# Optimization experiments

Hardware: AMD Instinct MI355X
Metric: run time of the kernel (lower is better)

## Reference

```python
import jax, jax.numpy as jnp
import numpy as np

B, S = 4, 128          # batch, seq
IN, OUT = 1024, 1024   # perfect squares
C = 256                # compressed_feature_dim
K = 4                  # num_monarchs
NI, NO = 32, 32        # sqrt(IN), sqrt(OUT)
D1 = NI * NI * NO      # flat size of M1 per token
D2 = NO * NI * NO      # flat size of M2 per token


def setup_inputs() -> dict:
    key = jax.random.key(0)
    ks = jax.random.split(key, 20)
    s = 0.02
    return {
        "x":   jax.random.normal(ks[0], (B, S, IN), dtype=jnp.float32),
        # compressor: Linear(IN, C)
        "Wc":  jax.random.normal(ks[1], (IN, C), dtype=jnp.float32) * s,
        "bc":  jnp.zeros((C,), dtype=jnp.float32),
        # M1 generators (stacked over K experts): Linear(C,C), SiLU, Linear(C,D1)
        "W1a": jax.random.normal(ks[2], (K, C, C), dtype=jnp.float32) * s,
        "b1a": jnp.zeros((K, C), dtype=jnp.float32),
        "W1b": jax.random.normal(ks[3], (K, C, D1), dtype=jnp.float32) * s,
        "b1b": jax.random.normal(ks[4], (K, D1), dtype=jnp.float32) * s,
        # M2 generators
        "W2a": jax.random.normal(ks[5], (K, C, C), dtype=jnp.float32) * s,
        "b2a": jnp.zeros((K, C), dtype=jnp.float32),
        "W2b": jax.random.normal(ks[6], (K, C, D2), dtype=jnp.float32) * s,
        "b2b": jax.random.normal(ks[7], (K, D2), dtype=jnp.float32) * s,
        # mixer: Linear(C,C), SiLU, Linear(C,K)
        "Wm1": jax.random.normal(ks[8], (C, C), dtype=jnp.float32) * s,
        "bm1": jnp.zeros((C,), dtype=jnp.float32),
        "Wm2": jax.random.normal(ks[9], (C, K), dtype=jnp.float32) * s,
        "bm2": jnp.zeros((K,), dtype=jnp.float32),
        # biasor: Linear(C, OUT)
        "Wb":  jax.random.normal(ks[10], (C, OUT), dtype=jnp.float32) * s,
        "bb":  jnp.zeros((OUT,), dtype=jnp.float32),
        # ratio_gen: Linear(C, 1)
        "Wr":  jax.random.normal(ks[11], (C, 1), dtype=jnp.float32) * s,
        "br":  jnp.ones((1,), dtype=jnp.float32),
    }


def reference(x, Wc, bc, W1a, b1a, W1b, b1b, W2a, b2a, W2b, b2b,
              Wm1, bm1, Wm2, bm2, Wb, bb, Wr, br):
    silu = jax.nn.silu
    # compressor
    c = silu(x @ Wc + bc)                                   # [B,S,C]
    # per-expert hypernetwork generation of flat Monarch factors
    h1 = silu(jnp.einsum('bsc,kcd->kbsd', c, W1a) + b1a[:, None, None, :])
    M1s = jnp.einsum('kbsd,kde->kbse', h1, W1b) + b1b[:, None, None, :]  # [K,B,S,D1]
    h2 = silu(jnp.einsum('bsc,kcd->kbsd', c, W2a) + b2a[:, None, None, :])
    M2s = jnp.einsum('kbsd,kde->kbse', h2, W2b) + b2b[:, None, None, :]  # [K,B,S,D2]
    # softmax mixing coefficients
    coeffs = jax.nn.softmax(silu(c @ Wm1 + bm1) @ Wm2 + bm2, axis=-1)    # [B,S,K]
    M1_flat = jnp.einsum('kbsd,bsk->bsd', M1s, coeffs)      # [B,S,D1]
    M2_flat = jnp.einsum('kbsd,bsk->bsd', M2s, coeffs)      # [B,S,D2]
    # per-token Monarch matmul
    lead = x.shape[:-1]
    M1 = M1_flat.reshape(*lead, NI, NI, NO)
    M2 = M2_flat.reshape(*lead, NO, NI, NO)
    x1 = x.reshape(*lead, NI, NI)                            # [B,S,g=NI,i=NI]
    x1o = jnp.einsum('bsgi,bsgio->bsgo', x1, M1)             # [B,S,NI,NO]
    x2 = jnp.swapaxes(x1o, -1, -2)                           # [B,S,NO,NI]
    x2o = jnp.einsum('bsgi,bsgio->bsgo', x2, M2)             # [B,S,NO,NO]
    y = x2o.reshape(*lead, NO * NO)                          # [B,S,OUT]
    ratio = c @ Wr + br                                      # [B,S,1]
    return y * ratio + (c @ Wb + bb)
```

## Files before the change

kernel.cpp:

```cpp
#include <hip/hip_runtime.h>


typedef __bf16 bf16x8 __attribute__((ext_vector_type(8)));
typedef __bf16 bf16x2 __attribute__((ext_vector_type(2)));
typedef float  fx4    __attribute__((ext_vector_type(4)));

#define NN 32768

__device__ __forceinline__ unsigned short f2bf(float f) {
  union { __bf16 b; unsigned short u; } c; c.b = (__bf16)f; return c.u;
}
__device__ __forceinline__ unsigned pk2(float lo, float hi) {
  bf16x2 v; v[0] = (__bf16)lo; v[1] = (__bf16)hi;
  union { bf16x2 v; unsigned u; } c; c.v = v; return c.u;
}
__device__ __forceinline__ float b2f(unsigned short s) {
  union { unsigned u; float f; } v; v.u = ((unsigned)s) << 16; return v.f;
}
__device__ __forceinline__ void up8(uint4 h, float* f) {
  f[0] = b2f((unsigned short)(h.x & 0xFFFF)); f[1] = b2f((unsigned short)(h.x >> 16));
  f[2] = b2f((unsigned short)(h.y & 0xFFFF)); f[3] = b2f((unsigned short)(h.y >> 16));
  f[4] = b2f((unsigned short)(h.z & 0xFFFF)); f[5] = b2f((unsigned short)(h.z >> 16));
  f[6] = b2f((unsigned short)(h.w & 0xFFFF)); f[7] = b2f((unsigned short)(h.w >> 16));
}
__device__ __forceinline__ uint4 scale8(uint4 h, float cv) {
  uint4 u;
  u.x = pk2(b2f((unsigned short)(h.x & 0xFFFF)) * cv, b2f((unsigned short)(h.x >> 16)) * cv);
  u.y = pk2(b2f((unsigned short)(h.y & 0xFFFF)) * cv, b2f((unsigned short)(h.y >> 16)) * cv);
  u.z = pk2(b2f((unsigned short)(h.z & 0xFFFF)) * cv, b2f((unsigned short)(h.z >> 16)) * cv);
  u.w = pk2(b2f((unsigned short)(h.w & 0xFFFF)) * cv, b2f((unsigned short)(h.w >> 16)) * cv);
  return u;
}
__device__ __forceinline__ float silu_f(float x) { return x / (1.f + __expf(-x)); }

__device__ __forceinline__ void gl2lds16(const void* g, void* l) {
  __builtin_amdgcn_global_load_lds(
      (const __attribute__((address_space(1))) unsigned int*)g,
      (__attribute__((address_space(3))) unsigned int*)l, 16, 0, 0);
}

#define MFMA(a, b, c) __builtin_amdgcn_mfma_f32_16x16x32_bf16((a), (b), (c), 0, 0, 0)

__global__ __launch_bounds__(256) void k1_compress(
    const float* __restrict__ x, const float* __restrict__ Wc,
    const float* __restrict__ bc, uint4* __restrict__ c_u4) {
  const int tid = threadIdx.x;
  const int m0 = blockIdx.x * 64, n0 = blockIdx.y * 64;
  __shared__ uint4 As[8 * 64];
  __shared__ uint4 Bs[8 * 65];
  const bf16x8* Af = reinterpret_cast<const bf16x8*>(As);
  const bf16x8* Bf = reinterpret_cast<const bf16x8*>(Bs);
  uint2* Bs2 = reinterpret_cast<uint2*>(Bs);
  const int lane = tid & 63, w = tid >> 6;
  const int q = lane >> 4, rr = lane & 15;
  const int wm = (w >> 1) * 32, wn = (w & 1) * 32;
  const int arun = tid & 7, amb = tid >> 3;
  const int kgrp = tid & 15, colg = tid >> 4;
  fx4 a00 = 0, a01 = 0, a10 = 0, a11 = 0;
  fx4 areg[4], breg[4];

#pragma unroll
  for (int s = 0; s < 2; ++s) {
    const float* src = x + (size_t)(m0 + amb + 32 * s) * 1024 + arun * 8;
    areg[2 * s] = *(const fx4*)src;
    areg[2 * s + 1] = *(const fx4*)(src + 4);
  }
#pragma unroll
  for (int kk = 0; kk < 4; ++kk)
    breg[kk] = *(const fx4*)(Wc + (size_t)(kgrp * 4 + kk) * 256 + n0 + colg * 4);

  for (int kt = 0; kt < 16; ++kt) {
    __syncthreads();
#pragma unroll
    for (int s = 0; s < 2; ++s) {
      uint4 u;
      u.x = pk2(areg[2 * s][0], areg[2 * s][1]);
      u.y = pk2(areg[2 * s][2], areg[2 * s][3]);
      u.z = pk2(areg[2 * s + 1][0], areg[2 * s + 1][1]);
      u.w = pk2(areg[2 * s + 1][2], areg[2 * s + 1][3]);
      As[arun * 64 + amb + 32 * s] = u;
    }
#pragma unroll
    for (int j = 0; j < 4; ++j) {
      uint2 u;
      u.x = pk2(breg[0][j], breg[1][j]);
      u.y = pk2(breg[2][j], breg[3][j]);
      Bs2[(((kgrp >> 1) * 65 + colg * 4 + j) << 1) + (kgrp & 1)] = u;
    }
    __syncthreads();
    if (kt < 15) {
      const int k0 = (kt + 1) * 64;
#pragma unroll
      for (int s = 0; s < 2; ++s) {
        const float* src = x + (size_t)(m0 + amb + 32 * s) * 1024 + k0 + arun * 8;
        areg[2 * s] = *(const fx4*)src;
        areg[2 * s + 1] = *(const fx4*)(src + 4);
      }
#pragma unroll
      for (int kk = 0; kk < 4; ++kk)
        breg[kk] = *(const fx4*)(Wc + (size_t)(k0 + kgrp * 4 + kk) * 256 + n0 + colg * 4);
    }
#pragma unroll
    for (int ks = 0; ks < 2; ++ks) {
      const int roA = (ks * 4 + q) * 64, roB = (ks * 4 + q) * 65;
      bf16x8 fa0 = Af[roA + wm + rr];
      bf16x8 fa1 = Af[roA + wm + 16 + rr];
      bf16x8 fb0 = Bf[roB + wn + rr];
      bf16x8 fb1 = Bf[roB + wn + 16 + rr];
      a00 = MFMA(fa0, fb0, a00); a01 = MFMA(fa0, fb1, a01);
      a10 = MFMA(fa1, fb0, a10); a11 = MFMA(fa1, fb1, a11);
    }
  }
  __syncthreads();
  {
    const int r4 = tid >> 6, m = tid & 63;
    uint4 u; u.x = (r4 == 0) ? 0x3F80u : 0u; u.y = 0; u.z = 0; u.w = 0;
    As[r4 * 64 + m] = u;
    uint4 ub; ub.x = (r4 == 0) ? (unsigned)f2bf(bc[n0 + m]) : 0u;
    ub.y = 0; ub.z = 0; ub.w = 0;
    Bs[r4 * 65 + m] = ub;
  }
  __syncthreads();
  {
    bf16x8 fa0 = Af[q * 64 + wm + rr];
    bf16x8 fa1 = Af[q * 64 + wm + 16 + rr];
    bf16x8 fb0 = Bf[q * 65 + wn + rr];
    bf16x8 fb1 = Bf[q * 65 + wn + 16 + rr];
    a00 = MFMA(fa0, fb0, a00); a01 = MFMA(fa0, fb1, a01);
    a10 = MFMA(fa1, fb0, a10); a11 = MFMA(fa1, fb1, a11);
  }
  unsigned short* c16 = (unsigned short*)c_u4;
#pragma unroll
  for (int fi = 0; fi < 2; ++fi) {
#pragma unroll
    for (int fj = 0; fj < 2; ++fj) {
      fx4 v = (fi == 0) ? (fj == 0 ? a00 : a01) : (fj == 0 ? a10 : a11);
      const int cc = n0 + wn + fj * 16 + rr;
#pragma unroll
      for (int reg = 0; reg < 4; ++reg) {
        const int t = m0 + wm + fi * 16 + q * 4 + reg;
        c16[((size_t)(cc >> 3) * 512 + t) * 8 + (cc & 7)] = f2bf(silu_f(v[reg]));
      }
    }
  }
  if (blockIdx.y == 0) {
    const int r4 = tid >> 6, m = tid & 63;
    uint4 u; u.x = (r4 == 0) ? 0x3F80u : 0u; u.y = 0; u.z = 0; u.w = 0;
    c_u4[(size_t)(32 + r4) * 512 + m0 + m] = u;
  }
}

__global__ __launch_bounds__(256) void k2_hyper(
    const uint4* __restrict__ c_u4,
    const float* __restrict__ W1a, const float* __restrict__ b1a,
    const float* __restrict__ W2a, const float* __restrict__ b2a,
    const float* __restrict__ Wm1, const float* __restrict__ bm1,
    const float* __restrict__ Wb, const float* __restrict__ bb,
    unsigned short* __restrict__ H, float* __restrict__ biasout) {
  const int tid = threadIdx.x;
  const int m0 = blockIdx.x * 64, n0 = blockIdx.y * 64;
  __shared__ uint4 As[2][8 * 64];
  __shared__ uint4 Bs[8 * 65];
  const bf16x8* Bf = reinterpret_cast<const bf16x8*>(Bs);
  uint2* Bs2 = reinterpret_cast<uint2*>(Bs);
  const int lane = tid & 63, w = tid >> 6;
  const int q = lane >> 4, rr = lane & 15;
  const int wm = (w >> 1) * 32, wn = (w & 1) * 32;
  const int kgrp = tid & 15, colg = tid >> 4;

  const float* bbase; const float* biasv; int bstride;
  if (n0 < 1024) {
    const int kx = n0 >> 8;
    bbase = W1a + (size_t)kx * 65536 + (n0 & 255); bstride = 256;
    biasv = b1a + kx * 256 + (n0 & 255);
  } else if (n0 < 2048) {
    const int mm = n0 - 1024; const int kx = mm >> 8;
    bbase = W2a + (size_t)kx * 65536 + (mm & 255); bstride = 256;
    biasv = b2a + kx * 256 + (mm & 255);
  } else if (n0 < 2304) {
    bbase = Wm1 + (n0 - 2048); bstride = 256; biasv = bm1 + (n0 - 2048);
  } else {
    bbase = Wb + (n0 - 2304); bstride = 1024; biasv = bb + (n0 - 2304);
  }

  fx4 a00 = 0, a01 = 0, a10 = 0, a11 = 0;
  fx4 breg[4];
#pragma unroll
  for (int kk = 0; kk < 4; ++kk)
    breg[kk] = *(const fx4*)(bbase + (size_t)(kgrp * 4 + kk) * bstride + colg * 4);
#pragma unroll
  for (int s = 0; s < 2; ++s) {
    const int run = w * 2 + s;
    gl2lds16(c_u4 + (size_t)run * 512 + m0 + lane, (void*)(&As[0][run * 64]));
  }
  int cur = 0;
  for (int kt = 0; kt < 4; ++kt) {
    __syncthreads();
#pragma unroll
    for (int j = 0; j < 4; ++j) {
      uint2 u;
      u.x = pk2(breg[0][j], breg[1][j]);
      u.y = pk2(breg[2][j], breg[3][j]);
      Bs2[(((kgrp >> 1) * 65 + colg * 4 + j) << 1) + (kgrp & 1)] = u;
    }
    __syncthreads();
    if (kt < 3) {
#pragma unroll
      for (int s = 0; s < 2; ++s) {
        const int run = w * 2 + s;
        gl2lds16(c_u4 + (size_t)((kt + 1) * 8 + run) * 512 + m0 + lane,
                 (void*)(&As[cur ^ 1][run * 64]));
      }
#pragma unroll
      for (int kk = 0; kk < 4; ++kk)
        breg[kk] = *(const fx4*)(bbase + (size_t)((kt + 1) * 64 + kgrp * 4 + kk) * bstride + colg * 4);
    }
    const bf16x8* Af = reinterpret_cast<const bf16x8*>(As[cur]);
#pragma unroll
    for (int ks = 0; ks < 2; ++ks) {
      const int roA = (ks * 4 + q) * 64, roB = (ks * 4 + q) * 65;
      bf16x8 fa0 = Af[roA + wm + rr];
      bf16x8 fa1 = Af[roA + wm + 16 + rr];
      bf16x8 fb0 = Bf[roB + wn + rr];
      bf16x8 fb1 = Bf[roB + wn + 16 + rr];
      a00 = MFMA(fa0, fb0, a00); a01 = MFMA(fa0, fb1, a01);
      a10 = MFMA(fa1, fb0, a10); a11 = MFMA(fa1, fb1, a11);
    }
    cur ^= 1;
  }
  __syncthreads();
  {
    gl2lds16(c_u4 + (size_t)(32 + w) * 512 + m0 + lane, (void*)(&As[0][w * 64]));
    const int r4 = tid >> 6, col = tid & 63;
    uint4 ub; ub.x = (r4 == 0) ? (unsigned)f2bf(biasv[col]) : 0u;
    ub.y = 0; ub.z = 0; ub.w = 0;
    Bs[r4 * 65 + col] = ub;
  }
  __syncthreads();
  {
    const bf16x8* Af = reinterpret_cast<const bf16x8*>(As[0]);
    bf16x8 fa0 = Af[q * 64 + wm + rr];
    bf16x8 fa1 = Af[q * 64 + wm + 16 + rr];
    bf16x8 fb0 = Bf[q * 65 + wn + rr];
    bf16x8 fb1 = Bf[q * 65 + wn + 16 + rr];
    a00 = MFMA(fa0, fb0, a00); a01 = MFMA(fa0, fb1, a01);
    a10 = MFMA(fa1, fb0, a10); a11 = MFMA(fa1, fb1, a11);
  }
#pragma unroll
  for (int fi = 0; fi < 2; ++fi) {
#pragma unroll
    for (int fj = 0; fj < 2; ++fj) {
      fx4 v = (fi == 0) ? (fj == 0 ? a00 : a01) : (fj == 0 ? a10 : a11);
      const int cc = n0 + wn + fj * 16 + rr;
#pragma unroll
      for (int reg = 0; reg < 4; ++reg) {
        const int t = m0 + wm + fi * 16 + q * 4 + reg;
        if (n0 < 2304)
          H[(((size_t)(cc >> 3) * 512 + t) << 3) + (cc & 7)] = f2bf(silu_f(v[reg]));
        else
          biasout[(size_t)t * 1024 + (cc - 2304)] = v[reg];
      }
    }
  }
}

__global__ __launch_bounds__(256) void k3_prep(
    const uint4* __restrict__ Hu, const uint4* __restrict__ c_u4,
    const float* __restrict__ Wm2, const float* __restrict__ bm2,
    const float* __restrict__ Wr, const float* __restrict__ br,
    uint4* __restrict__ G1u, uint4* __restrict__ G2u, float* __restrict__ ratio) {
  const int tid = threadIdx.x;
  const int tg = blockIdx.x & 7, dgrp = blockIdx.x >> 3;
  const int t0 = tg * 64;
  __shared__ float sWm2[1024];
  __shared__ float sWr[256];
  __shared__ float part[64][4][4];
  __shared__ float rp[64][4];
  __shared__ float cf[64][4];
  ((fx4*)sWm2)[tid] = ((const fx4*)Wm2)[tid];
  if (tid < 64) ((fx4*)sWr)[tid] = ((const fx4*)Wr)[tid];
  __syncthreads();
  const int tl = tid >> 2, kx = tid & 3;
  {
    float pe0 = 0, pe1 = 0, pe2 = 0, pe3 = 0, pr = 0;
#pragma unroll
    for (int i = 0; i < 8; ++i) {
      uint4 h  = Hu[(size_t)(256 + kx * 8 + i) * 512 + t0 + tl];
      uint4 cu = c_u4[(size_t)(kx * 8 + i) * 512 + t0 + tl];
      float hf[8], cv[8];
      up8(h, hf); up8(cu, cv);
#pragma unroll
      for (int j = 0; j < 8; ++j) {
        const int ch = kx * 64 + i * 8 + j;
        pe0 += hf[j] * sWm2[ch * 4 + 0];
        pe1 += hf[j] * sWm2[ch * 4 + 1];
        pe2 += hf[j] * sWm2[ch * 4 + 2];
        pe3 += hf[j] * sWm2[ch * 4 + 3];
        pr  += cv[j] * sWr[ch];
      }
    }
    part[tl][kx][0] = pe0; part[tl][kx][1] = pe1;
    part[tl][kx][2] = pe2; part[tl][kx][3] = pe3;
    rp[tl][kx] = pr;
  }
  __syncthreads();
  if (tid < 64) {
    float l[4];
#pragma unroll
    for (int e = 0; e < 4; ++e)
      l[e] = part[tid][0][e] + part[tid][1][e] + part[tid][2][e] + part[tid][3][e] + bm2[e];
    float m = fmaxf(fmaxf(l[0], l[1]), fmaxf(l[2], l[3]));
    float e0 = __expf(l[0] - m), e1 = __expf(l[1] - m);
    float e2 = __expf(l[2] - m), e3 = __expf(l[3] - m);
    float den = e0 + e1 + e2 + e3;
    cf[tid][0] = e0 / den; cf[tid][1] = e1 / den;
    cf[tid][2] = e2 / den; cf[tid][3] = e3 / den;
    if (dgrp == 0)
      ratio[t0 + tid] = rp[tid][0] + rp[tid][1] + rp[tid][2] + rp[tid][3] + br[0];
  }
  __syncthreads();
  const int tl2 = tid & 63, sub = tid >> 6;
#pragma unroll
  for (int i = 0; i < 4; ++i) {
    const int dg = dgrp * 16 + sub * 4 + i;
    const float cv = cf[tl2][dg >> 5];
    uint4 h1 = Hu[(size_t)dg * 512 + t0 + tl2];
    G1u[(size_t)dg * 512 + t0 + tl2] = scale8(h1, cv);
    uint4 h2 = Hu[(size_t)(128 + dg) * 512 + t0 + tl2];
    G2u[(size_t)dg * 512 + t0 + tl2] = scale8(h2, cv);
  }
  if (dgrp == 0) {
    if (tid < 64) {
      uint4 u;
      u.x = pk2(cf[tid][0], cf[tid][1]);
      u.y = pk2(cf[tid][2], cf[tid][3]);
      u.z = 0; u.w = 0;
      G1u[(size_t)128 * 512 + t0 + tid] = u;
      G2u[(size_t)128 * 512 + t0 + tid] = u;
    } else {
      const int idx = tid - 64;
      uint4 z; z.x = 0; z.y = 0; z.z = 0; z.w = 0;
      G1u[(size_t)(129 + (idx >> 6)) * 512 + t0 + (idx & 63)] = z;
      G2u[(size_t)(129 + (idx >> 6)) * 512 + t0 + (idx & 63)] = z;
    }
  }
}

__global__ __launch_bounds__(256) void k_biggemm(
    const uint4* __restrict__ Gu, const float* __restrict__ W,
    const float* __restrict__ bvec, unsigned short* __restrict__ Mout) {
  const int tid = threadIdx.x;
  const int p = blockIdx.x;
  const int xcd = p & 7, slot = p >> 3;
  const int m0 = (slot & 3) * 128;
  const int n0 = ((slot >> 2) * 8 + xcd) * 128;
  __shared__ uint4 Bs[2][8 * 129];
  const int lane = tid & 63, w = tid >> 6;
  const int q = lane >> 4, rr = lane & 15;
  const int wm = (w >> 1) * 64, wn = (w & 1) * 64;
  const int bcg = tid >> 3;
  const int br  = tid & 7;
  const float* wptr = W + n0 + bcg * 4;
  const uint4* aptr = Gu + m0 + wm + rr;

  fx4 acc[4][4];
#pragma unroll
  for (int i = 0; i < 4; ++i)
#pragma unroll
    for (int j = 0; j < 4; ++j) acc[i][j] = 0;

  fx4 breg[8];
  uint4 a_cur[4], a_nxt[4];
#pragma unroll
  for (int kk = 0; kk < 8; ++kk)
    breg[kk] = *(const fx4*)(wptr + (size_t)(br * 8 + kk) * NN);
#pragma unroll
  for (int j = 0; j < 4; ++j) {
    uint4 u;
    u.x = pk2(breg[0][j], breg[1][j]); u.y = pk2(breg[2][j], breg[3][j]);
    u.z = pk2(breg[4][j], breg[5][j]); u.w = pk2(breg[6][j], breg[7][j]);
    Bs[0][br * 129 + bcg * 4 + j] = u;
  }
#pragma unroll
  for (int kk = 0; kk < 8; ++kk)
    breg[kk] = *(const fx4*)(wptr + (size_t)(64 + br * 8 + kk) * NN);
#pragma unroll
  for (int f = 0; f < 4; ++f) a_cur[f] = aptr[(size_t)q * 512 + f * 16];
  __syncthreads();

  for (int kt = 0; kt < 16; ++kt) {
    const int cur = kt & 1;
    const bf16x8* Bf = reinterpret_cast<const bf16x8*>(Bs[cur]);
    if (kt < 15) {
#pragma unroll
      for (int j = 0; j < 4; ++j) {
        uint4 u;
        u.x = pk2(breg[0][j], breg[1][j]); u.y = pk2(breg[2][j], breg[3][j]);
        u.z = pk2(breg[4][j], breg[5][j]); u.w = pk2(breg[6][j], breg[7][j]);
        Bs[cur ^ 1][br * 129 + bcg * 4 + j] = u;
      }
      if (kt < 14) {
#pragma unroll
        for (int kk = 0; kk < 8; ++kk)
          breg[kk] = *(const fx4*)(wptr + (size_t)((kt + 2) * 64 + br * 8 + kk) * NN);
      }
    }
#pragma unroll
    for (int ks = 0; ks < 2; ++ks) {
      if (kt < 15 || ks < 1) {
        const int nk8 = (ks == 0) ? (kt * 8 + 4 + q) : ((kt + 1) * 8 + q);
#pragma unroll
        for (int f = 0; f < 4; ++f) a_nxt[f] = aptr[(size_t)nk8 * 512 + f * 16];
      }
      bf16x8 b[4];
      const int roB = (ks * 4 + q) * 129;
#pragma unroll
      for (int f = 0; f < 4; ++f) b[f] = Bf[roB + wn + f * 16 + rr];
#pragma unroll
      for (int fi = 0; fi < 4; ++fi) {
        bf16x8 af = *reinterpret_cast<bf16x8*>(&a_cur[fi]);
#pragma unroll
        for (int fj = 0; fj < 4; ++fj) acc[fi][fj] = MFMA(af, b[fj], acc[fi][fj]);
      }
#pragma unroll
      for (int f = 0; f < 4; ++f) a_cur[f] = a_nxt[f];
    }
    __syncthreads();
  }
  {
#pragma unroll
    for (int f = 0; f < 4; ++f) a_cur[f] = aptr[(size_t)(128 + q) * 512 + f * 16];
    const int colB = tid & 127, half = tid >> 7;
    if (half == 0) {
#pragma unroll
      for (int r = 0; r < 4; ++r) {
        float v8[8];
#pragma unroll
        for (int j = 0; j < 8; ++j) {
          const int kk = r * 8 + j;
          v8[j] = (kk < 4) ? bvec[(size_t)kk * NN + n0 + colB] : 0.f;
        }
        uint4 u; u.x = pk2(v8[0], v8[1]); u.y = pk2(v8[2], v8[3]);
        u.z = pk2(v8[4], v8[5]); u.w = pk2(v8[6], v8[7]);
        Bs[0][r * 129 + colB] = u;
      }
    }
    __syncthreads();
    const bf16x8* Bf0 = reinterpret_cast<const bf16x8*>(Bs[0]);
    bf16x8 b[4];
#pragma unroll
    for (int f = 0; f < 4; ++f) b[f] = Bf0[q * 129 + wn + f * 16 + rr];
#pragma unroll
    for (int fi = 0; fi < 4; ++fi) {
      bf16x8 af = *reinterpret_cast<bf16x8*>(&a_cur[fi]);
#pragma unroll
      for (int fj = 0; fj < 4; ++fj) acc[fi][fj] = MFMA(af, b[fj], acc[fi][fj]);
    }
  }
#pragma unroll
  for (int fi = 0; fi < 4; ++fi) {
    const int tb = m0 + wm + fi * 16 + q * 4;
#pragma unroll
    for (int fj = 0; fj < 4; ++fj) {
      const fx4 v = acc[fi][fj];
      const int cc = n0 + wn + fj * 16 + rr;
      const int pc = ((cc >> 5) & 31) * 1024 + (cc >> 10) * 32 + (cc & 31);
#pragma unroll
      for (int reg = 0; reg < 4; ++reg)
        Mout[(size_t)(tb + reg) * NN + pc] = f2bf(v[reg]);
    }
  }
}

__global__ __launch_bounds__(256) void k_monarch1(
    const float* __restrict__ x, const unsigned short* __restrict__ M1p,
    float* __restrict__ XT) {
  const int tt = blockIdx.x, tid = threadIdx.x;
  const int h = tid >> 7, t2 = tid & 127;
  __shared__ float xs[1024];
  __shared__ float xo[2][1024];
  *(float4*)&xs[tid * 4] = *(const float4*)&x[(size_t)tt * 1024 + tid * 4];
  __syncthreads();
  const int g = t2 >> 2, ob = (t2 & 3) * 8;
  const unsigned short* mrow =
      M1p + (size_t)tt * NN + (size_t)h * 16 * 1024 + g * 32 + ob;
  float acc[8] = {0, 0, 0, 0, 0, 0, 0, 0};
#pragma unroll
  for (int i = 0; i < 16; ++i) {
    uint4 mv = *(const uint4*)&mrow[(size_t)i * 1024];
    float mf[8]; up8(mv, mf);
    const float xv = xs[g * 32 + h * 16 + i];
#pragma unroll
    for (int j = 0; j < 8; ++j) acc[j] += xv * mf[j];
  }
#pragma unroll
  for (int j = 0; j < 8; ++j) xo[h][(ob + j) * 32 + g] = acc[j];
  __syncthreads();
  {
    const int base = tid * 4;
    float4 v0 = *(const float4*)&xo[0][base];
    float4 v1 = *(const float4*)&xo[1][base];
    float4 o; o.x = v0.x + v1.x; o.y = v0.y + v1.y;
    o.z = v0.z + v1.z; o.w = v0.w + v1.w;
    *(float4*)&XT[(size_t)tt * 1024 + base] = o;
  }
}

__global__ __launch_bounds__(256) void k_monarch2(
    const unsigned short* __restrict__ M2p, const float* __restrict__ XT,
    const float* __restrict__ biasout, const float* __restrict__ ratio,
    float* __restrict__ out) {
  const int tt = blockIdx.x, tid = threadIdx.x;
  const int h = tid >> 7, t2 = tid & 127;
  __shared__ float xs[1024];
  __shared__ float xo[2][1024];
  *(float4*)&xs[tid * 4] = *(const float4*)&XT[(size_t)tt * 1024 + tid * 4];
  __syncthreads();
  const int g = t2 >> 2, ob = (t2 & 3) * 8;
  const unsigned short* mrow =
      M2p + (size_t)tt * NN + (size_t)h * 16 * 1024 + g * 32 + ob;
  float acc[8] = {0, 0, 0, 0, 0, 0, 0, 0};
#pragma unroll
  for (int i = 0; i < 16; ++i) {
    uint4 mv = *(const uint4*)&mrow[(size_t)i * 1024];
    float mf[8]; up8(mv, mf);
    const float xv = xs[g * 32 + h * 16 + i];
#pragma unroll
    for (int j = 0; j < 8; ++j) acc[j] += xv * mf[j];
  }
#pragma unroll
  for (int j = 0; j < 8; ++j) xo[h][g * 32 + ob + j] = acc[j];
  __syncthreads();
  {
    const float r = ratio[tt];
    const int base = tid * 4;
    float4 v0 = *(const float4*)&xo[0][base];
    float4 v1 = *(const float4*)&xo[1][base];
    float4 bo = *(const float4*)&biasout[(size_t)tt * 1024 + base];
    float4 o;
    o.x = (v0.x + v1.x) * r + bo.x; o.y = (v0.y + v1.y) * r + bo.y;
    o.z = (v0.z + v1.z) * r + bo.z; o.w = (v0.w + v1.w) * r + bo.w;
    *(float4*)&out[(size_t)tt * 1024 + base] = o;
  }
}

extern "C" void kernel_launch(void* const* d_in, const int* in_sizes, int n_in,
                              void* d_out, int out_size, void* d_ws, size_t ws_size,
                              hipStream_t stream) {
  (void)in_sizes; (void)n_in; (void)out_size; (void)ws_size;
  const float* x   = (const float*)d_in[0];
  const float* Wc  = (const float*)d_in[1];
  const float* bc  = (const float*)d_in[2];
  const float* W1a = (const float*)d_in[3];
  const float* b1a = (const float*)d_in[4];
  const float* W1b = (const float*)d_in[5];
  const float* b1b = (const float*)d_in[6];
  const float* W2a = (const float*)d_in[7];
  const float* b2a = (const float*)d_in[8];
  const float* W2b = (const float*)d_in[9];
  const float* b2b = (const float*)d_in[10];
  const float* Wm1 = (const float*)d_in[11];
  const float* bm1 = (const float*)d_in[12];
  const float* Wm2 = (const float*)d_in[13];
  const float* bm2 = (const float*)d_in[14];
  const float* Wb  = (const float*)d_in[15];
  const float* bb  = (const float*)d_in[16];
  const float* Wr  = (const float*)d_in[17];
  const float* br  = (const float*)d_in[18];
  float* out = (float*)d_out;

  char* ws = (char*)d_ws;
  uint4* c_u4            = (uint4*)(ws + 0);
  unsigned short* H      = (unsigned short*)(ws + 294912);
  float* biasout         = (float*)(ws + 2654208);
  uint4* G1u             = (uint4*)(ws + 4751360);
  uint4* G2u             = (uint4*)(ws + 5832704);
  float* ratio           = (float*)(ws + 6914048);
  float* XT              = (float*)(ws + 6918144);
  unsigned short* M      = (unsigned short*)(ws + 9015296);

  k1_compress<<<dim3(8, 4), 256, 0, stream>>>(x, Wc, bc, c_u4);
  k2_hyper<<<dim3(8, 52), 256, 0, stream>>>(c_u4, W1a, b1a, W2a, b2a, Wm1, bm1,
                                            Wb, bb, H, biasout);
  k3_prep<<<64, 256, 0, stream>>>((const uint4*)H, c_u4, Wm2, bm2, Wr, br,
                                  G1u, G2u, ratio);
  k_biggemm<<<1024, 256, 0, stream>>>(G1u, W1b, b1b, M);
  k_monarch1<<<512, 256, 0, stream>>>(x, M, XT);
  k_biggemm<<<1024, 256, 0, stream>>>(G2u, W2b, b2b, M);
  k_monarch2<<<512, 256, 0, stream>>>(M, XT, biasout, ratio, out);
}
```

Baseline: 468.6 us.

## Pre-convert generator weights to bf16 in piggybacked blocks, use direct-to-LDS loads in biggemm

The fp32-to-bf16 packing of W1b/W2b (and their biases) moves out of the big GEMM into extra blocks appended to k1_compress and k_monarch1. Those blocks write a pre-packed bf16 workspace Wt that the GEMM then streams with global_load_lds. The GEMM loses its register-staged B pipeline and the in-loop conversions, and each K step now loads A and B tiles straight into LDS between two barriers. The trade-off is an extra full write and read of the converted weights each call, plus a GEMM with no software double-buffering.

```diff
diff --git a/kernel.cpp b/kernel.cpp
--- a/kernel.cpp
+++ b/kernel.cpp
@@ -41,11 +41,43 @@
 
 #define MFMA(a, b, c) __builtin_amdgcn_mfma_f32_16x16x32_bf16((a), (b), (c), 0, 0, 0)
 
+__device__ __forceinline__ void wconv_body(int cb, const float* __restrict__ W,
+                                           const float* __restrict__ bvec,
+                                           uint4* __restrict__ Wt) {
+  const int ur = cb >> 5;
+  const int n0 = (cb & 31) * 1024 + threadIdx.x * 4;
+  fx4 r[8];
+  if (ur < 128) {
+#pragma unroll
+    for (int kk = 0; kk < 8; ++kk)
+      r[kk] = *(const fx4*)(W + (size_t)(ur * 8 + kk) * NN + n0);
+  } else {
+#pragma unroll
+    for (int kk = 0; kk < 8; ++kk) r[kk] = 0;
+    if (ur == 128) {
+#pragma unroll
+      for (int kk = 0; kk < 4; ++kk)
+        r[kk] = *(const fx4*)(bvec + (size_t)kk * NN + n0);
+    }
+  }
+#pragma unroll
+  for (int j = 0; j < 4; ++j) {
+    uint4 u;
+    u.x = pk2(r[0][j], r[1][j]); u.y = pk2(r[2][j], r[3][j]);
+    u.z = pk2(r[4][j], r[5][j]); u.w = pk2(r[6][j], r[7][j]);
+    Wt[(size_t)ur * NN + n0 + j] = u;
+  }
+}
+
 __global__ __launch_bounds__(256) void k1_compress(
     const float* __restrict__ x, const float* __restrict__ Wc,
-    const float* __restrict__ bc, uint4* __restrict__ c_u4) {
+    const float* __restrict__ bc, uint4* __restrict__ c_u4,
+    const float* __restrict__ W1b, const float* __restrict__ b1b,
+    uint4* __restrict__ Wt) {
+  const int b = blockIdx.x;
+  if (b >= 32) { wconv_body(b - 32, W1b, b1b, Wt); return; }
   const int tid = threadIdx.x;
-  const int m0 = blockIdx.x * 64, n0 = blockIdx.y * 64;
+  const int m0 = (b & 7) * 64, n0 = (b >> 3) * 64;
   __shared__ uint4 As[8 * 64];
   __shared__ uint4 Bs[8 * 65];
   const bf16x8* Af = reinterpret_cast<const bf16x8*>(As);
@@ -143,7 +175,7 @@
       }
     }
   }
-  if (blockIdx.y == 0) {
+  if ((b >> 3) == 0) {
     const int r4 = tid >> 6, m = tid & 63;
     uint4 u; u.x = (r4 == 0) ? 0x3F80u : 0u; u.y = 0; u.z = 0; u.w = 0;
     c_u4[(size_t)(32 + r4) * 512 + m0 + m] = u;
@@ -347,21 +379,20 @@
 }
 
 __global__ __launch_bounds__(256) void k_biggemm(
-    const uint4* __restrict__ Gu, const float* __restrict__ W,
-    const float* __restrict__ bvec, unsigned short* __restrict__ Mout) {
+    const uint4* __restrict__ Gu, const uint4* __restrict__ Wt,
+    unsigned short* __restrict__ Mout) {
   const int tid = threadIdx.x;
   const int p = blockIdx.x;
   const int xcd = p & 7, slot = p >> 3;
   const int m0 = (slot & 3) * 128;
   const int n0 = ((slot >> 2) * 8 + xcd) * 128;
-  __shared__ uint4 Bs[2][8 * 129];
+  __shared__ uint4 As[8 * 128];
+  __shared__ uint4 Bs[8 * 128];
+  const bf16x8* Af = reinterpret_cast<const bf16x8*>(As);
+  const bf16x8* Bf = reinterpret_cast<const bf16x8*>(Bs);
   const int lane = tid & 63, w = tid >> 6;
   const int q = lane >> 4, rr = lane & 15;
   const int wm = (w >> 1) * 64, wn = (w & 1) * 64;
-  const int bcg = tid >> 3;
-  const int br  = tid & 7;
-  const float* wptr = W + n0 + bcg * 4;
-  const uint4* aptr = Gu + m0 + wm + rr;
 
   fx4 acc[4][4];
 #pragma unroll
@@ -369,93 +400,56 @@
 #pragma unroll
     for (int j = 0; j < 4; ++j) acc[i][j] = 0;
 
-  fx4 breg[8];
-  uint4 a_cur[4], a_nxt[4];
-#pragma unroll
-  for (int kk = 0; kk < 8; ++kk)
-    breg[kk] = *(const fx4*)(wptr + (size_t)(br * 8 + kk) * NN);
-#pragma unroll
-  for (int j = 0; j < 4; ++j) {
-    uint4 u;
-    u.x = pk2(breg[0][j], breg[1][j]); u.y = pk2(breg[2][j], breg[3][j]);
-    u.z = pk2(breg[4][j], breg[5][j]); u.w = pk2(breg[6][j], breg[7][j]);
-    Bs[0][br * 129 + bcg * 4 + j] = u;
-  }
-#pragma unroll
-  for (int kk = 0; kk < 8; ++kk)
-    breg[kk] = *(const fx4*)(wptr + (size_t)(64 + br * 8 + kk) * NN);
-#pragma unroll
-  for (int f = 0; f < 4; ++f) a_cur[f] = aptr[(size_t)q * 512 + f * 16];
-  __syncthreads();
-
   for (int kt = 0; kt < 16; ++kt) {
-    const int cur = kt & 1;
-    const bf16x8* Bf = reinterpret_cast<const bf16x8*>(Bs[cur]);
-    if (kt < 15) {
-#pragma unroll
-      for (int j = 0; j < 4; ++j) {
-        uint4 u;
-        u.x = pk2(breg[0][j], breg[1][j]); u.y = pk2(breg[2][j], breg[3][j]);
-        u.z = pk2(breg[4][j], breg[5][j]); u.w = pk2(breg[6][j], breg[7][j]);
-        Bs[cur ^ 1][br * 129 + bcg * 4 + j] = u;
+    __syncthreads();
+#pragma unroll
+    for (int s = 0; s < 4; ++s) {
+      const int idx = w * 4 + s;
+      const int run = idx >> 1, hf = (idx & 1) * 64;
+      gl2lds16(Gu + (size_t)(kt * 8 + run) * 512 + m0 + hf + lane,
+               (void*)(&As[run * 128 + hf]));
+      gl2lds16(Wt + (size_t)(kt * 8 + run) * NN + n0 + hf + lane,
+               (void*)(&Bs[run * 128 + hf]));
+    }
+    __syncthreads();
+#pragma unroll
+    for (int ks = 0; ks < 2; ++ks) {
+      const int ro = (ks * 4 + q) * 128;
+      bf16x8 a[4], b[4];
+#pragma unroll
+      for (int f = 0; f < 4; ++f) {
+        a[f] = Af[ro + wm + f * 16 + rr];
+        b[f] = Bf[ro + wn + f * 16 + rr];
       }
-      if (kt < 14) {
-#pragma unroll
-        for (int kk = 0; kk < 8; ++kk)
-          breg[kk] = *(const fx4*)(wptr + (size_t)((kt + 2) * 64 + br * 8 + kk) * NN);
-      }
-    }
-#pragma unroll
-    for (int ks = 0; ks < 2; ++ks) {
-      if (kt < 15 || ks < 1) {
-        const int nk8 = (ks == 0) ? (kt * 8 + 4 + q) : ((kt + 1) * 8 + q);
-#pragma unroll
-        for (int f = 0; f < 4; ++f) a_nxt[f] = aptr[(size_t)nk8 * 512 + f * 16];
-      }
-      bf16x8 b[4];
-      const int roB = (ks * 4 + q) * 129;
-#pragma unroll
-      for (int f = 0; f < 4; ++f) b[f] = Bf[roB + wn + f * 16 + rr];
-#pragma unroll
-      for (int fi = 0; fi < 4; ++fi) {
-        bf16x8 af = *reinterpret_cast<bf16x8*>(&a_cur[fi]);
-#pragma unroll
-        for (int fj = 0; fj < 4; ++fj) acc[fi][fj] = MFMA(af, b[fj], acc[fi][fj]);
-      }
-#pragma unroll
-      for (int f = 0; f < 4; ++f) a_cur[f] = a_nxt[f];
-    }
-    __syncthreads();
-  }
-  {
-#pragma unroll
-    for (int f = 0; f < 4; ++f) a_cur[f] = aptr[(size_t)(128 + q) * 512 + f * 16];
-    const int colB = tid & 127, half = tid >> 7;
-    if (half == 0) {
-#pragma unroll
-      for (int r = 0; r < 4; ++r) {
-        float v8[8];
-#pragma unroll
-        for (int j = 0; j < 8; ++j) {
-          const int kk = r * 8 + j;
-          v8[j] = (kk < 4) ? bvec[(size_t)kk * NN + n0 + colB] : 0.f;
-        }
-        uint4 u; u.x = pk2(v8[0], v8[1]); u.y = pk2(v8[2], v8[3]);
-        u.z = pk2(v8[4], v8[5]); u.w = pk2(v8[6], v8[7]);
-        Bs[0][r * 129 + colB] = u;
-      }
-    }
-    __syncthreads();
-    const bf16x8* Bf0 = reinterpret_cast<const bf16x8*>(Bs[0]);
-    bf16x8 b[4];
-#pragma unroll
-    for (int f = 0; f < 4; ++f) b[f] = Bf0[q * 129 + wn + f * 16 + rr];
-#pragma unroll
-    for (int fi = 0; fi < 4; ++fi) {
-      bf16x8 af = *reinterpret_cast<bf16x8*>(&a_cur[fi]);
-#pragma unroll
-      for (int fj = 0; fj < 4; ++fj) acc[fi][fj] = MFMA(af, b[fj], acc[fi][fj]);
-    }
+#pragma unroll
+      for (int fi = 0; fi < 4; ++fi)
+#pragma unroll
+        for (int fj = 0; fj < 4; ++fj) acc[fi][fj] = MFMA(a[fi], b[fj], acc[fi][fj]);
+    }
+  }
+  __syncthreads();
+#pragma unroll
+  for (int s = 0; s < 2; ++s) {
+    const int idx = w * 2 + s;
+    const int run = idx >> 1, hf = (idx & 1) * 64;
+    gl2lds16(Gu + (size_t)(128 + run) * 512 + m0 + hf + lane,
+             (void*)(&As[run * 128 + hf]));
+    gl2lds16(Wt + (size_t)(128 + run) * NN + n0 + hf + lane,
+             (void*)(&Bs[run * 128 + hf]));
+  }
+  __syncthreads();
+  {
+    const int ro = q * 128;
+    bf16x8 a[4], b[4];
+#pragma unroll
+    for (int f = 0; f < 4; ++f) {
+      a[f] = Af[ro + wm + f * 16 + rr];
+      b[f] = Bf[ro + wn + f * 16 + rr];
+    }
+#pragma unroll
+    for (int fi = 0; fi < 4; ++fi)
+#pragma unroll
+      for (int fj = 0; fj < 4; ++fj) acc[fi][fj] = MFMA(a[fi], b[fj], acc[fi][fj]);
   }
 #pragma unroll
   for (int fi = 0; fi < 4; ++fi) {
@@ -474,8 +468,12 @@
 
 __global__ __launch_bounds__(256) void k_monarch1(
     const float* __restrict__ x, const unsigned short* __restrict__ M1p,
-    float* __restrict__ XT) {
-  const int tt = blockIdx.x, tid = threadIdx.x;
+    float* __restrict__ XT,
+    const float* __restrict__ W2b, const float* __restrict__ b2b,
+    uint4* __restrict__ Wt) {
+  const int b = blockIdx.x;
+  if (b >= 512) { wconv_body(b - 512, W2b, b2b, Wt); return; }
+  const int tt = b, tid = threadIdx.x;
   const int h = tid >> 7, t2 = tid & 127;
   __shared__ float xs[1024];
   __shared__ float xo[2][1024];
@@ -578,14 +576,15 @@
   float* ratio           = (float*)(ws + 6914048);
   float* XT              = (float*)(ws + 6918144);
   unsigned short* M      = (unsigned short*)(ws + 9015296);
-
-  k1_compress<<<dim3(8, 4), 256, 0, stream>>>(x, Wc, bc, c_u4);
+  uint4* Wt              = (uint4*)(ws + 42569728);
+
+  k1_compress<<<4256, 256, 0, stream>>>(x, Wc, bc, c_u4, W1b, b1b, Wt);
   k2_hyper<<<dim3(8, 52), 256, 0, stream>>>(c_u4, W1a, b1a, W2a, b2a, Wm1, bm1,
                                             Wb, bb, H, biasout);
   k3_prep<<<64, 256, 0, stream>>>((const uint4*)H, c_u4, Wm2, bm2, Wr, br,
                                   G1u, G2u, ratio);
-  k_biggemm<<<1024, 256, 0, stream>>>(G1u, W1b, b1b, M);
-  k_monarch1<<<512, 256, 0, stream>>>(x, M, XT);
-  k_biggemm<<<1024, 256, 0, stream>>>(G2u, W2b, b2b, M);
+  k_biggemm<<<1024, 256, 0, stream>>>(G1u, Wt, M);
+  k_monarch1<<<4736, 256, 0, stream>>>(x, M, XT, W2b, b2b, Wt);
+  k_biggemm<<<1024, 256, 0, stream>>>(G2u, Wt, M);
   k_monarch2<<<512, 256, 0, stream>>>(M, XT, biasout, ratio, out);
 }
```

Result: faster. 441.2 us (-5.8%).
